# Kernel optimization log

Measured on AMD Instinct MI355X. Metric: run time of the kernel, lower is better.

The kernel has to match this reference:

```python
import jax, jax.numpy as jnp
import numpy as np

B, C, H, W = 2, 512, 64, 64
GROUPS = 32
EPS = 1e-6


def setup_inputs() -> dict:
    key = jax.random.key(0)
    ks = jax.random.split(key, 9)
    s = 1.0 / np.sqrt(C)
    return {
        "x": jax.random.normal(ks[0], (B, C, H, W), dtype=jnp.float32),
        "gamma": jnp.ones((C,), dtype=jnp.float32),
        "beta": jnp.zeros((C,), dtype=jnp.float32),
        "wq": jax.random.normal(ks[1], (C, C), dtype=jnp.float32) * s,
        "bq": jnp.zeros((C,), dtype=jnp.float32),
        "wk": jax.random.normal(ks[2], (C, C), dtype=jnp.float32) * s,
        "bk": jnp.zeros((C,), dtype=jnp.float32),
        "wv": jax.random.normal(ks[3], (C, C), dtype=jnp.float32) * s,
        "bv": jnp.zeros((C,), dtype=jnp.float32),
        "wp": jax.random.normal(ks[4], (C, C), dtype=jnp.float32) * s,
        "bp": jnp.zeros((C,), dtype=jnp.float32),
    }


def _group_norm(x, gamma, beta):
    b, c, h, w = x.shape
    xg = x.reshape(b, GROUPS, c // GROUPS, h, w)
    mean = jnp.mean(xg, axis=(2, 3, 4), keepdims=True)
    var = jnp.var(xg, axis=(2, 3, 4), keepdims=True)
    xn = ((xg - mean) * jax.lax.rsqrt(var + EPS)).reshape(b, c, h, w)
    return xn * gamma[None, :, None, None] + beta[None, :, None, None]


def reference(x, gamma, beta, wq, bq, wk, bk, wv, bv, wp, bp):
    b, c, h, w = x.shape
    hn = _group_norm(x, gamma, beta)
    # 1x1 convs == per-pixel linear; flatten spatial: (b, hw, c)
    t = hn.reshape(b, c, h * w).transpose(0, 2, 1)
    q = jnp.einsum('bnc,oc->bno', t, wq) + bq
    k = jnp.einsum('bnc,oc->bno', t, wk) + bk
    v = jnp.einsum('bnc,oc->bno', t, wv) + bv
    scale = float(int(c) ** (-0.5))
    attn = jax.nn.softmax(jnp.einsum('bic,bjc->bij', q, k) * scale, axis=-1)
    o = jnp.einsum('bij,bjc->bic', attn, v)  # (b, hw, c)
    o = jnp.einsum('bnc,oc->bno', o, wp) + bp
    o = o.transpose(0, 2, 1).reshape(b, c, h, w)
    return x + o
```

## Files before the change

### kernel.cpp

```cpp
#include <hip/hip_runtime.h>
#include <hip/hip_bf16.h>

#define B_ 2
#define C_ 512
#define HW_ 4096
#define K_ 512
#define EPS_ 1e-6f
#define SCALE_ 0.04419417382415922f
#define NEG_INF_ (-1e30f)

typedef __attribute__((ext_vector_type(8))) __bf16 bf16x8;
typedef __attribute__((ext_vector_type(4))) float f32x4;
typedef __attribute__((ext_vector_type(16))) float f32x16;

__device__ __forceinline__ unsigned short f2bf(float f) {
  union { float f; unsigned u; } v; v.f = f;
  unsigned r = v.u + 0x7fffu + ((v.u >> 16) & 1u);
  return (unsigned short)(r >> 16);
}
__device__ __forceinline__ float bf2f(unsigned short h) {
  union { unsigned u; float f; } v; v.u = ((unsigned)h) << 16;
  return v.f;
}

__device__ __forceinline__ void gld_lds16(const unsigned short* g, unsigned short* l) {
  __builtin_amdgcn_global_load_lds((const __attribute__((address_space(1))) void*)g,
                                   (__attribute__((address_space(3))) void*)l, 16, 0, 0);
}

__global__ void gn_sums(const float* __restrict__ x, float* __restrict__ stats) {
  int bid = blockIdx.x;
  int bg = bid >> 4, row = bid & 15;
  int b = bg >> 5, g = bg & 31;
  const float* base = x + ((size_t)(b * C_ + g * 16 + row)) * HW_;
  float s = 0.f, s2 = 0.f;
  int t = threadIdx.x;
  #pragma unroll
  for (int i = 0; i < 4; ++i) {
    float4 v = *reinterpret_cast<const float4*>(base + (size_t)(t + i * 256) * 4);
    s  += v.x + v.y + v.z + v.w;
    s2 += v.x * v.x + v.y * v.y + v.z * v.z + v.w * v.w;
  }
  for (int off = 32; off; off >>= 1) { s += __shfl_down(s, off); s2 += __shfl_down(s2, off); }
  __shared__ float rs[4], rs2[4];
  int w = t >> 6;
  if ((t & 63) == 0) { rs[w] = s; rs2[w] = s2; }
  __syncthreads();
  if (t == 0) {
    atomicAdd(&stats[bg], rs[0] + rs[1] + rs[2] + rs[3]);
    atomicAdd(&stats[64 + bg], rs2[0] + rs2[1] + rs2[2] + rs2[3]);
  }
}

__global__ void build_t(const float* __restrict__ x, const float* __restrict__ stats,
                        const float* __restrict__ gamma, const float* __restrict__ beta,
                        unsigned short* __restrict__ tb) {
  __shared__ float lds[64 * 69];
  int n0 = blockIdx.x * 64, c0 = blockIdx.y * 64, b = blockIdx.z;
  int t = threadIdx.x;
  {
    int cl = t >> 2, ch = t & 3;
    int c = c0 + cl;
    int bg = b * 32 + (c >> 4);
    float s = stats[bg], s2v = stats[64 + bg];
    float mean = s * (1.f / 65536.f);
    float var = s2v * (1.f / 65536.f) - mean * mean;
    float rstd = rsqrtf(var + EPS_);
    float ga = gamma[c] * rstd;
    float be = beta[c] - mean * ga;
    const float* xr = x + ((size_t)(b * C_ + c)) * HW_ + n0 + ch * 16;
    #pragma unroll
    for (int i = 0; i < 4; ++i) {
      float4 v = *reinterpret_cast<const float4*>(xr + i * 4);
      int nl = ch * 16 + i * 4;
      lds[cl * 69 + nl + 0] = v.x * ga + be;
      lds[cl * 69 + nl + 1] = v.y * ga + be;
      lds[cl * 69 + nl + 2] = v.z * ga + be;
      lds[cl * 69 + nl + 3] = v.w * ga + be;
    }
  }
  __syncthreads();
  {
    int nl = t >> 2, cw = t & 3;
    unsigned short* orow = tb + ((size_t)(b * HW_ + n0 + nl)) * C_ + c0 + cw * 16;
    #pragma unroll
    for (int i = 0; i < 4; ++i) {
      ushort4 o4;
      o4.x = f2bf(lds[(cw * 16 + i * 4 + 0) * 69 + nl]);
      o4.y = f2bf(lds[(cw * 16 + i * 4 + 1) * 69 + nl]);
      o4.z = f2bf(lds[(cw * 16 + i * 4 + 2) * 69 + nl]);
      o4.w = f2bf(lds[(cw * 16 + i * 4 + 3) * 69 + nl]);
      *reinterpret_cast<ushort4*>(orow + i * 4) = o4;
    }
  }
}

__global__ void cast_w4(const float* __restrict__ s0, const float* __restrict__ s1,
                        const float* __restrict__ s2, const float* __restrict__ s3,
                        unsigned short* __restrict__ dst) {
  int which = blockIdx.y;
  const float* src = which == 0 ? s0 : which == 1 ? s1 : which == 2 ? s2 : s3;
  int i = (blockIdx.x * 256 + threadIdx.x) * 4;
  float4 v = *reinterpret_cast<const float4*>(src + i);
  ushort4 o; o.x = f2bf(v.x); o.y = f2bf(v.y); o.z = f2bf(v.z); o.w = f2bf(v.w);
  *reinterpret_cast<ushort4*>(dst + (size_t)which * 262144 + i) = o;
}

__global__ __launch_bounds__(256, 2) void gemm_qkv(
    const unsigned short* __restrict__ tb, const unsigned short* __restrict__ wqkv,
    const float* __restrict__ bq, const float* __restrict__ bk, const float* __restrict__ bv,
    unsigned short* __restrict__ qb, unsigned short* __restrict__ kb,
    unsigned short* __restrict__ vTb) {
  __shared__ unsigned short Al[2][128 * 64];
  __shared__ unsigned short Bl[2][128 * 64];
  int z = blockIdx.z;
  int which = z >> 1, b = z & 1;
  const unsigned short* Ab = (which < 2) ? (tb + (size_t)b * HW_ * K_) : (wqkv + 2 * 262144);
  const unsigned short* Bb = (which < 2) ? (wqkv + which * 262144) : (tb + (size_t)b * HW_ * K_);
  int m0 = (which < 2) ? blockIdx.y * 128 : blockIdx.x * 128;
  int n0 = (which < 2) ? blockIdx.x * 128 : blockIdx.y * 128;
  int N = (which < 2) ? 512 : HW_;
  unsigned short* Cb = (which == 0) ? (qb + (size_t)b * HW_ * K_)
                     : (which == 1) ? (kb + (size_t)b * HW_ * K_)
                                    : (vTb + (size_t)b * C_ * HW_);
  const float* bias = (which == 0) ? bq : (which == 1) ? bk : bv;
  int t = threadIdx.x, lane = t & 63, w = t >> 6;
  int l15 = lane & 15, quad = lane >> 4;
  int mw = (w & 1) * 64, nw = (w >> 1) * 64;
  int sr8 = lane >> 3, sb = lane & 7;
  f32x4 acc[4][4] = {};

  #define G_STAGE(KC) do {                                                          \
    int pb = (KC) & 1;                                                              \
    _Pragma("unroll")                                                               \
    for (int q = 0; q < 4; ++q) {                                                   \
      int row = w * 32 + q * 8 + sr8;                                               \
      int gb = sb ^ (row & 7);                                                      \
      gld_lds16(Ab + (size_t)(m0 + row) * K_ + (KC) * 64 + gb * 8, &Al[pb][(w * 32 + q * 8) * 64]); \
      gld_lds16(Bb + (size_t)(n0 + row) * K_ + (KC) * 64 + gb * 8, &Bl[pb][(w * 32 + q * 8) * 64]); \
    }                                                                               \
  } while (0)

  G_STAGE(0);
  __syncthreads();
  for (int kc = 0; kc < 8; ++kc) {
    if (kc < 7) G_STAGE(kc + 1);
    const unsigned short* Ac = Al[kc & 1];
    const unsigned short* Bc = Bl[kc & 1];
    #pragma unroll
    for (int kk = 0; kk < 2; ++kk) {
      bf16x8 af[4];
      #pragma unroll
      for (int mt = 0; mt < 4; ++mt)
        af[mt] = *reinterpret_cast<const bf16x8*>(
            &Ac[(mw + mt * 16 + l15) * 64 + (((kk * 4 + quad) ^ (l15 & 7)) << 3)]);
      #pragma unroll
      for (int nt = 0; nt < 4; ++nt) {
        bf16x8 bfr = *reinterpret_cast<const bf16x8*>(
            &Bc[(nw + nt * 16 + l15) * 64 + (((kk * 4 + quad) ^ (l15 & 7)) << 3)]);
        #pragma unroll
        for (int mt = 0; mt < 4; ++mt)
          acc[mt][nt] = __builtin_amdgcn_mfma_f32_16x16x32_bf16(af[mt], bfr, acc[mt][nt], 0, 0, 0);
      }
    }
    __syncthreads();
  }
  #undef G_STAGE
  #pragma unroll
  for (int mt = 0; mt < 4; ++mt)
    #pragma unroll
    for (int nt = 0; nt < 4; ++nt)
      #pragma unroll
      for (int rr = 0; rr < 4; ++rr) {
        int row = m0 + mw + mt * 16 + quad * 4 + rr;
        int col = n0 + nw + nt * 16 + l15;
        float v = acc[mt][nt][rr] + ((which < 2) ? bias[col] : bias[row]);
        Cb[(size_t)row * N + col] = f2bf(v);
      }
}

template <int MODE>
__global__ __launch_bounds__(256, 2) void gemm_bt(
    const unsigned short* __restrict__ A, long sA,
    const unsigned short* __restrict__ B, long sB,
    void* __restrict__ Cv, long sC, int M, int N,
    const float* __restrict__ bias,
    const float* __restrict__ resid, long sR) {
  __shared__ unsigned short Al[2][128 * 64];
  __shared__ unsigned short Bl[2][128 * 64];
  int z = blockIdx.z;
  const unsigned short* Ab = A + (size_t)z * sA;
  const unsigned short* Bb = B + (size_t)z * sB;
  int n0 = blockIdx.x * 128, m0 = blockIdx.y * 128;
  int t = threadIdx.x, lane = t & 63, w = t >> 6;
  int l15 = lane & 15, quad = lane >> 4;
  int mw = (w & 1) * 64, nw = (w >> 1) * 64;
  int sr8 = lane >> 3, sb = lane & 7;
  f32x4 acc[4][4] = {};

  #define G_STAGE(KC) do {                                                          \
    int pb = (KC) & 1;                                                              \
    _Pragma("unroll")                                                               \
    for (int q = 0; q < 4; ++q) {                                                   \
      int row = w * 32 + q * 8 + sr8;                                               \
      int gb = sb ^ (row & 7);                                                      \
      gld_lds16(Ab + (size_t)(m0 + row) * K_ + (KC) * 64 + gb * 8, &Al[pb][(w * 32 + q * 8) * 64]); \
      gld_lds16(Bb + (size_t)(n0 + row) * K_ + (KC) * 64 + gb * 8, &Bl[pb][(w * 32 + q * 8) * 64]); \
    }                                                                               \
  } while (0)

  G_STAGE(0);
  __syncthreads();
  for (int kc = 0; kc < 8; ++kc) {
    if (kc < 7) G_STAGE(kc + 1);
    const unsigned short* Ac = Al[kc & 1];
    const unsigned short* Bc = Bl[kc & 1];
    #pragma unroll
    for (int kk = 0; kk < 2; ++kk) {
      bf16x8 af[4];
      #pragma unroll
      for (int mt = 0; mt < 4; ++mt)
        af[mt] = *reinterpret_cast<const bf16x8*>(
            &Ac[(mw + mt * 16 + l15) * 64 + (((kk * 4 + quad) ^ (l15 & 7)) << 3)]);
      #pragma unroll
      for (int nt = 0; nt < 4; ++nt) {
        bf16x8 bfr = *reinterpret_cast<const bf16x8*>(
            &Bc[(nw + nt * 16 + l15) * 64 + (((kk * 4 + quad) ^ (l15 & 7)) << 3)]);
        #pragma unroll
        for (int mt = 0; mt < 4; ++mt)
          acc[mt][nt] = __builtin_amdgcn_mfma_f32_16x16x32_bf16(af[mt], bfr, acc[mt][nt], 0, 0, 0);
      }
    }
    __syncthreads();
  }
  #undef G_STAGE
  #pragma unroll
  for (int mt = 0; mt < 4; ++mt)
    #pragma unroll
    for (int nt = 0; nt < 4; ++nt)
      #pragma unroll
      for (int rr = 0; rr < 4; ++rr) {
        int row = m0 + mw + mt * 16 + quad * 4 + rr;
        int col = n0 + nw + nt * 16 + l15;
        float v = acc[mt][nt][rr];
        if (MODE == 0) {
          v += bias[col];
          reinterpret_cast<unsigned short*>(Cv)[(size_t)z * sC + (size_t)row * N + col] = f2bf(v);
        } else if (MODE == 1) {
          v += bias[row];
          reinterpret_cast<unsigned short*>(Cv)[(size_t)z * sC + (size_t)row * N + col] = f2bf(v);
        } else {
          v += bias[row];
          v += resid[(size_t)z * sR + (size_t)row * N + col];
          reinterpret_cast<float*>(Cv)[(size_t)z * sC + (size_t)row * N + col] = v;
        }
      }
}

__global__ __launch_bounds__(512, 2) void attn(
    const unsigned short* __restrict__ qg, const unsigned short* __restrict__ kg,
    const unsigned short* __restrict__ vg,
    unsigned short* __restrict__ opart, float* __restrict__ mpart, float* __restrict__ lpart) {
  __shared__ unsigned short KVb[2 * 16384];
  __shared__ unsigned short Pl[64 * 264];
  __shared__ float sm_m[64], sm_l[64], sm_alpha[64], sm_red[128];
  int qt = blockIdx.x, jh = blockIdx.y, b = blockIdx.z;
  int t = threadIdx.x, lane = t & 63, w = t >> 6;
  int l15 = lane & 15, quad = lane >> 4;
  int l31 = lane & 31, hl = lane >> 5;
  int rw = w & 3, cw = w >> 2;
  int rw2 = w & 1, dg = w >> 1;
  int m0 = qt * 64;
  if (t < 64) { sm_m[t] = NEG_INF_; sm_l[t] = 0.f; }

  int st_r[4], st_kb[4];
  #pragma unroll
  for (int q = 0; q < 4; ++q) {
    int blk = w * 4 + q;
    st_r[q] = blk * 4 + (lane >> 4);
    st_kb[q] = (lane & 15) ^ (st_r[q] & 7);
  }

  #define STAGE_K(JC, KC, J0) do {                                                  \
    const unsigned short* gb = kg + ((size_t)(b * HW_ + (J0) + (JC) * 128)) * K_ + (KC) * 128; \
    unsigned short* lb = KVb + ((((JC) * 4 + (KC)) & 1) << 14);                     \
    _Pragma("unroll")                                                               \
    for (int q = 0; q < 4; ++q)                                                     \
      gld_lds16(gb + (size_t)st_r[q] * K_ + st_kb[q] * 8, lb + (w * 4 + q) * 512);  \
  } while (0)

  #define STAGE_V(DC, JC, J0) do {                                                 \
    const unsigned short* gb = vg + ((size_t)(b * K_ + (DC) * 128)) * HW_ + (J0) + (JC) * 128; \
    unsigned short* lb = KVb + (((DC) & 1) << 14);                                  \
    _Pragma("unroll")                                                               \
    for (int q = 0; q < 4; ++q)                                                     \
      gld_lds16(gb + (size_t)st_r[q] * HW_ + st_kb[q] * 8, lb + (w * 4 + q) * 512); \
  } while (0)

  bf16x8 qa[16];
  {
    const unsigned short* qrow = qg + ((size_t)(b * HW_ + m0 + rw * 16 + l15)) * K_ + quad * 8;
    #pragma unroll
    for (int kk = 0; kk < 16; ++kk)
      qa[kk] = *reinterpret_cast<const bf16x8*>(qrow + kk * 32);
  }
  f32x16 acc_o[4] = {};

  int j0 = jh * 2048;
  STAGE_K(0, 0, j0);
  __syncthreads();

  for (int it = 0; it < 8; ++it, j0 += 256) {
    f32x4 acc_s[8] = {};
    #pragma unroll
    for (int c = 0; c < 8; ++c) {
      int jc = c >> 2, kc = c & 3;
      if (c < 7) { STAGE_K((c + 1) >> 2, (c + 1) & 3, j0); }
      else       { STAGE_V(0, 0, j0); }
      const unsigned short* bufc = KVb + ((c & 1) << 14);
      #pragma unroll
      for (int kk = 0; kk < 4; ++kk)
        #pragma unroll
        for (int ct = 0; ct < 4; ++ct) {
          int jr = cw * 64 + ct * 16 + l15;
          bf16x8 bfr = *reinterpret_cast<const bf16x8*>(
              &bufc[jr * 128 + (((kk * 4 + quad) ^ (l15 & 7)) << 3)]);
          acc_s[jc * 4 + ct] = __builtin_amdgcn_mfma_f32_16x16x32_bf16(qa[kc * 4 + kk], bfr, acc_s[jc * 4 + ct], 0, 0, 0);
        }
      __syncthreads();
    }
    float mx[4];
    #pragma unroll
    for (int rr = 0; rr < 4; ++rr) {
      float m = NEG_INF_;
      #pragma unroll
      for (int s = 0; s < 8; ++s) {
        acc_s[s][rr] *= SCALE_;
        m = fmaxf(m, acc_s[s][rr]);
      }
      mx[rr] = m;
    }
    #pragma unroll
    for (int off = 1; off < 16; off <<= 1)
      #pragma unroll
      for (int rr = 0; rr < 4; ++rr)
        mx[rr] = fmaxf(mx[rr], __shfl_xor(mx[rr], off));
    if (l15 == 0)
      #pragma unroll
      for (int rr = 0; rr < 4; ++rr)
        sm_red[cw * 64 + rw * 16 + quad * 4 + rr] = mx[rr];
    __syncthreads();
    if (t < 64) {
      float mnew = fmaxf(sm_m[t], fmaxf(sm_red[t], sm_red[64 + t]));
      sm_alpha[t] = __expf(sm_m[t] - mnew);
      sm_m[t] = mnew;
    }
    __syncthreads();
    float sum[4] = {0.f, 0.f, 0.f, 0.f};
    #pragma unroll
    for (int s = 0; s < 8; ++s)
      #pragma unroll
      for (int rr = 0; rr < 4; ++rr) {
        int rowl = rw * 16 + quad * 4 + rr;
        float p = __expf(acc_s[s][rr] - sm_m[rowl]);
        sum[rr] += p;
        Pl[rowl * 264 + (s >> 2) * 128 + cw * 64 + (s & 3) * 16 + l15] = f2bf(p);
      }
    #pragma unroll
    for (int off = 1; off < 16; off <<= 1)
      #pragma unroll
      for (int rr = 0; rr < 4; ++rr)
        sum[rr] += __shfl_xor(sum[rr], off);
    if (l15 == 0)
      #pragma unroll
      for (int rr = 0; rr < 4; ++rr)
        sm_red[cw * 64 + rw * 16 + quad * 4 + rr] = sum[rr];
    __syncthreads();
    if (t < 64)
      sm_l[t] = sm_l[t] * sm_alpha[t] + sm_red[t] + sm_red[64 + t];
    #pragma unroll
    for (int r16 = 0; r16 < 16; ++r16) {
      int row = rw2 * 32 + (r16 & 3) + 8 * (r16 >> 2) + 4 * hl;
      float a = sm_alpha[row];
      #pragma unroll
      for (int dc = 0; dc < 4; ++dc)
        acc_o[dc][r16] *= a;
    }
    bf16x8 pa_r[8];
    #pragma unroll
    for (int c = 0; c < 8; ++c) {
      int jc = c >> 2, dc = c & 3;
      if ((c & 3) == 0) {
        #pragma unroll
        for (int ksx = 0; ksx < 8; ++ksx)
          pa_r[ksx] = *reinterpret_cast<const bf16x8*>(
              &Pl[(rw2 * 32 + l31) * 264 + jc * 128 + ksx * 16 + hl * 8]);
      }
      if (c < 7)          { STAGE_V((c + 1) & 3, (c + 1) >> 2, j0); }
      else if (it < 7)    { STAGE_K(0, 0, j0 + 256); }
      const unsigned short* bufc = KVb + ((c & 1) << 14);
      #pragma unroll
      for (int ksx = 0; ksx < 8; ++ksx) {
        bf16x8 vb = *reinterpret_cast<const bf16x8*>(
            &bufc[(dg * 32 + l31) * 128 + (((ksx * 2 + hl) ^ (l31 & 7)) << 3)]);
        acc_o[dc] = __builtin_amdgcn_mfma_f32_32x32x16_bf16(pa_r[ksx], vb, acc_o[dc], 0, 0, 0);
      }
      __syncthreads();
    }
  }
  #undef STAGE_K
  #undef STAGE_V
  int part = jh * 2 + b;
  unsigned short* ob = opart + ((size_t)part * HW_ + m0) * 512;
  #pragma unroll
  for (int dc = 0; dc < 4; ++dc) {
    int d = dc * 128 + dg * 32 + l31;
    #pragma unroll
    for (int r16 = 0; r16 < 16; ++r16) {
      int row = rw2 * 32 + (r16 & 3) + 8 * (r16 >> 2) + 4 * hl;
      ob[(size_t)row * 512 + d] = f2bf(acc_o[dc][r16]);
    }
  }
  if (t < 64) {
    mpart[(size_t)part * HW_ + m0 + t] = sm_m[t];
    lpart[(size_t)part * HW_ + m0 + t] = sm_l[t];
  }
}

__global__ void merge_o(const unsigned short* __restrict__ opart, const float* __restrict__ mpart,
                        const float* __restrict__ lpart, unsigned short* __restrict__ om) {
  int rg = blockIdx.x;
  int b = rg >> 12, n = rg & 4095;
  float m[2], l[2], M = NEG_INF_;
  #pragma unroll
  for (int p = 0; p < 2; ++p) {
    size_t r = (size_t)(p * 2 + b) * HW_ + n;
    m[p] = mpart[r]; l[p] = lpart[r];
    M = fmaxf(M, m[p]);
  }
  float wgt[2], L = 0.f;
  #pragma unroll
  for (int p = 0; p < 2; ++p) { wgt[p] = __expf(m[p] - M); L += l[p] * wgt[p]; }
  float inv = 1.f / L;
  unsigned short* orow = om + (size_t)rg * 512;
  for (int d = threadIdx.x; d < 512; d += 256) {
    float acc = 0.f;
    #pragma unroll
    for (int p = 0; p < 2; ++p)
      acc += bf2f(opart[((size_t)(p * 2 + b) * HW_ + n) * 512 + d]) * wgt[p];
    orow[d] = f2bf(acc * inv);
  }
}

extern "C" void kernel_launch(void* const* d_in, const int* in_sizes, int n_in,
                              void* d_out, int out_size, void* d_ws, size_t ws_size,
                              hipStream_t stream) {
  const float* x     = (const float*)d_in[0];
  const float* gamma = (const float*)d_in[1];
  const float* beta  = (const float*)d_in[2];
  const float* wq    = (const float*)d_in[3];
  const float* bq    = (const float*)d_in[4];
  const float* wk    = (const float*)d_in[5];
  const float* bk    = (const float*)d_in[6];
  const float* wv    = (const float*)d_in[7];
  const float* bv    = (const float*)d_in[8];
  const float* wp    = (const float*)d_in[9];
  const float* bp    = (const float*)d_in[10];
  float* out = (float*)d_out;

  char* ws = (char*)d_ws;
  size_t o = 0;
  float* stats          = (float*)(ws + o);          o += 1024;
  unsigned short* tb    = (unsigned short*)(ws + o); o += 8388608;
  unsigned short* qb    = (unsigned short*)(ws + o); o += 8388608;
  unsigned short* kb    = (unsigned short*)(ws + o); o += 8388608;
  unsigned short* vTb   = (unsigned short*)(ws + o); o += 8388608;
  unsigned short* wqb   = (unsigned short*)(ws + o); o += 524288;
  unsigned short* wkb   = (unsigned short*)(ws + o); o += 524288;
  unsigned short* wvb   = (unsigned short*)(ws + o); o += 524288;
  unsigned short* wpb   = (unsigned short*)(ws + o); o += 524288;
  unsigned short* opart = (unsigned short*)(ws + o); o += 16777216;
  float* mpart          = (float*)(ws + o);          o += 65536;
  float* lpart          = (float*)(ws + o);          o += 65536;
  unsigned short* om    = tb;

  hipMemsetAsync(stats, 0, 512, stream);
  gn_sums<<<1024, 256, 0, stream>>>(x, stats);
  build_t<<<dim3(64, 8, 2), 256, 0, stream>>>(x, stats, gamma, beta, tb);
  cast_w4<<<dim3(256, 4), 256, 0, stream>>>(wq, wk, wv, wp, wqb);
  gemm_qkv<<<dim3(4, 32, 6), 256, 0, stream>>>(tb, wqb, bq, bk, bv, qb, kb, vTb);
  attn<<<dim3(64, 2, 2), 512, 0, stream>>>(qb, kb, vTb, opart, mpart, lpart);
  merge_o<<<8192, 256, 0, stream>>>(opart, mpart, lpart, om);
  gemm_bt<2><<<dim3(32, 4, 2), 256, 0, stream>>>(wpb, 0, om, (long)HW_ * K_, out, (long)C_ * HW_, C_, HW_, bp, x, (long)C_ * HW_);
}
```

Before: 279.6 us.

## Merge weight cast into GN stats kernel, add MFMA priority, vectorize merge

Folds the four-weight bf16 cast into the group-norm sum kernel as extra blocks, removing one kernel launch. It also raises wave priority around the MFMA loops in the attention kernel so matrix work is favoured over staging loads. Finally, merge_o now has each thread handle two adjacent bf16 outputs with 32-bit loads and stores instead of looping over scalars. The effects are small and the setprio change may not help, since scheduling gains depend on how waves interleave.

```diff
diff --git a/kernel.cpp b/kernel.cpp
--- a/kernel.cpp
+++ b/kernel.cpp
@@ -28,27 +28,40 @@
                                    (__attribute__((address_space(3))) void*)l, 16, 0, 0);
 }
 
-__global__ void gn_sums(const float* __restrict__ x, float* __restrict__ stats) {
+__global__ void gn_cast(const float* __restrict__ x, float* __restrict__ stats,
+                        const float* __restrict__ s0, const float* __restrict__ s1,
+                        const float* __restrict__ s2, const float* __restrict__ s3,
+                        unsigned short* __restrict__ dst) {
   int bid = blockIdx.x;
-  int bg = bid >> 4, row = bid & 15;
-  int b = bg >> 5, g = bg & 31;
-  const float* base = x + ((size_t)(b * C_ + g * 16 + row)) * HW_;
-  float s = 0.f, s2 = 0.f;
   int t = threadIdx.x;
-  #pragma unroll
-  for (int i = 0; i < 4; ++i) {
-    float4 v = *reinterpret_cast<const float4*>(base + (size_t)(t + i * 256) * 4);
-    s  += v.x + v.y + v.z + v.w;
-    s2 += v.x * v.x + v.y * v.y + v.z * v.z + v.w * v.w;
-  }
-  for (int off = 32; off; off >>= 1) { s += __shfl_down(s, off); s2 += __shfl_down(s2, off); }
-  __shared__ float rs[4], rs2[4];
-  int w = t >> 6;
-  if ((t & 63) == 0) { rs[w] = s; rs2[w] = s2; }
-  __syncthreads();
-  if (t == 0) {
-    atomicAdd(&stats[bg], rs[0] + rs[1] + rs[2] + rs[3]);
-    atomicAdd(&stats[64 + bg], rs2[0] + rs2[1] + rs2[2] + rs2[3]);
+  if (bid < 1024) {
+    int bg = bid >> 4, row = bid & 15;
+    int b = bg >> 5, g = bg & 31;
+    const float* base = x + ((size_t)(b * C_ + g * 16 + row)) * HW_;
+    float s = 0.f, s2 = 0.f;
+    #pragma unroll
+    for (int i = 0; i < 4; ++i) {
+      float4 v = *reinterpret_cast<const float4*>(base + (size_t)(t + i * 256) * 4);
+      s  += v.x + v.y + v.z + v.w;
+      s2 += v.x * v.x + v.y * v.y + v.z * v.z + v.w * v.w;
+    }
+    for (int off = 32; off; off >>= 1) { s += __shfl_down(s, off); s2 += __shfl_down(s2, off); }
+    __shared__ float rs[4], rs2[4];
+    int w = t >> 6;
+    if ((t & 63) == 0) { rs[w] = s; rs2[w] = s2; }
+    __syncthreads();
+    if (t == 0) {
+      atomicAdd(&stats[bg], rs[0] + rs[1] + rs[2] + rs[3]);
+      atomicAdd(&stats[64 + bg], rs2[0] + rs2[1] + rs2[2] + rs2[3]);
+    }
+  } else {
+    int cid = bid - 1024;
+    int which = cid >> 8, bx = cid & 255;
+    const float* src = which == 0 ? s0 : which == 1 ? s1 : which == 2 ? s2 : s3;
+    int i = (bx * 256 + t) * 4;
+    float4 v = *reinterpret_cast<const float4*>(src + i);
+    ushort4 o; o.x = f2bf(v.x); o.y = f2bf(v.y); o.z = f2bf(v.z); o.w = f2bf(v.w);
+    *reinterpret_cast<ushort4*>(dst + (size_t)which * 262144 + i) = o;
   }
 }
 
@@ -93,17 +106,6 @@
       *reinterpret_cast<ushort4*>(orow + i * 4) = o4;
     }
   }
-}
-
-__global__ void cast_w4(const float* __restrict__ s0, const float* __restrict__ s1,
-                        const float* __restrict__ s2, const float* __restrict__ s3,
-                        unsigned short* __restrict__ dst) {
-  int which = blockIdx.y;
-  const float* src = which == 0 ? s0 : which == 1 ? s1 : which == 2 ? s2 : s3;
-  int i = (blockIdx.x * 256 + threadIdx.x) * 4;
-  float4 v = *reinterpret_cast<const float4*>(src + i);
-  ushort4 o; o.x = f2bf(v.x); o.y = f2bf(v.y); o.z = f2bf(v.z); o.w = f2bf(v.w);
-  *reinterpret_cast<ushort4*>(dst + (size_t)which * 262144 + i) = o;
 }
 
 __global__ __launch_bounds__(256, 2) void gemm_qkv(
@@ -318,6 +320,7 @@
       if (c < 7) { STAGE_K((c + 1) >> 2, (c + 1) & 3, j0); }
       else       { STAGE_V(0, 0, j0); }
       const unsigned short* bufc = KVb + ((c & 1) << 14);
+      __builtin_amdgcn_s_setprio(1);
       #pragma unroll
       for (int kk = 0; kk < 4; ++kk)
         #pragma unroll
@@ -327,6 +330,7 @@
               &bufc[jr * 128 + (((kk * 4 + quad) ^ (l15 & 7)) << 3)]);
           acc_s[jc * 4 + ct] = __builtin_amdgcn_mfma_f32_16x16x32_bf16(qa[kc * 4 + kk], bfr, acc_s[jc * 4 + ct], 0, 0, 0);
         }
+      __builtin_amdgcn_s_setprio(0);
       __syncthreads();
     }
     float mx[4];
@@ -399,12 +403,14 @@
       if (c < 7)          { STAGE_V((c + 1) & 3, (c + 1) >> 2, j0); }
       else if (it < 7)    { STAGE_K(0, 0, j0 + 256); }
       const unsigned short* bufc = KVb + ((c & 1) << 14);
+      __builtin_amdgcn_s_setprio(1);
       #pragma unroll
       for (int ksx = 0; ksx < 8; ++ksx) {
         bf16x8 vb = *reinterpret_cast<const bf16x8*>(
             &bufc[(dg * 32 + l31) * 128 + (((ksx * 2 + hl) ^ (l31 & 7)) << 3)]);
         acc_o[dc] = __builtin_amdgcn_mfma_f32_32x32x16_bf16(pa_r[ksx], vb, acc_o[dc], 0, 0, 0);
       }
+      __builtin_amdgcn_s_setprio(0);
       __syncthreads();
     }
   }
@@ -442,14 +448,17 @@
   #pragma unroll
   for (int p = 0; p < 2; ++p) { wgt[p] = __expf(m[p] - M); L += l[p] * wgt[p]; }
   float inv = 1.f / L;
-  unsigned short* orow = om + (size_t)rg * 512;
-  for (int d = threadIdx.x; d < 512; d += 256) {
-    float acc = 0.f;
-    #pragma unroll
-    for (int p = 0; p < 2; ++p)
-      acc += bf2f(opart[((size_t)(p * 2 + b) * HW_ + n) * 512 + d]) * wgt[p];
-    orow[d] = f2bf(acc * inv);
-  }
+  int d = threadIdx.x * 2;
+  float a0 = 0.f, a1 = 0.f;
+  #pragma unroll
+  for (int p = 0; p < 2; ++p) {
+    unsigned u = *reinterpret_cast<const unsigned*>(
+        &opart[((size_t)(p * 2 + b) * HW_ + n) * 512 + d]);
+    a0 += bf2f((unsigned short)(u & 0xffffu)) * wgt[p];
+    a1 += bf2f((unsigned short)(u >> 16)) * wgt[p];
+  }
+  unsigned out = (unsigned)f2bf(a0 * inv) | ((unsigned)f2bf(a1 * inv) << 16);
+  *reinterpret_cast<unsigned*>(om + (size_t)rg * 512 + d) = out;
 }
 
 extern "C" void kernel_launch(void* const* d_in, const int* in_sizes, int n_in,
@@ -485,9 +494,8 @@
   unsigned short* om    = tb;
 
   hipMemsetAsync(stats, 0, 512, stream);
-  gn_sums<<<1024, 256, 0, stream>>>(x, stats);
+  gn_cast<<<2048, 256, 0, stream>>>(x, stats, wq, wk, wv, wp, wqb);
   build_t<<<dim3(64, 8, 2), 256, 0, stream>>>(x, stats, gamma, beta, tb);
-  cast_w4<<<dim3(256, 4), 256, 0, stream>>>(wq, wk, wv, wp, wqb);
   gemm_qkv<<<dim3(4, 32, 6), 256, 0, stream>>>(tb, wqb, bq, bk, bv, qb, kb, vTb);
   attn<<<dim3(64, 2, 2), 512, 0, stream>>>(qb, kb, vTb, opart, mpart, lpart);
   merge_o<<<8192, 256, 0, stream>>>(opart, mpart, lpart, om);
```

After: 271.5 us. 2.9% less time.
